# Kernel tuning notes

Measured on AMD Instinct MI355X. Metric: run time of the kernel, lower is better.

## Reference

```python
import jax, jax.numpy as jnp
import numpy as np

N_ITEMS = 30000
N_HOPS = 2
TMP = 0.2
EPS = 1e-12


def _l2norm(x):
    # F.normalize(x, dim=1): x / max(||x||_2, eps)
    n = jnp.sqrt(jnp.sum(x * x, axis=1, keepdims=True))
    return x / jnp.maximum(n, EPS)


def setup_inputs() -> dict:
    key = jax.random.key(0)
    ks = jax.random.split(key, 12)
    n_users, n_entities, n_items, d = 50000, 100000, N_ITEMS, 64
    n_rel, n_fac, n_cls = 16, 4, 8
    n_edges, n_inter = 1000000, 500000
    return {
        'user_emb': jax.random.normal(ks[0], (n_users, d), jnp.float32),
        'entity_emb': jax.random.normal(ks[1], (n_entities, d), jnp.float32),
        'cls_emb': jax.random.normal(ks[2], (n_cls, d), jnp.float32),
        'latent_emb': jax.random.normal(ks[3], (n_fac, d), jnp.float32),
        'relation_emb': jax.random.normal(ks[4], (n_rel, d), jnp.float32),
        'disen_weight_att': jax.random.normal(ks[5], (n_fac, n_rel), jnp.float32),
        'edge_index': jax.random.randint(ks[6], (2, n_edges), 0, n_entities, jnp.int32),
        'edge_type': jax.random.randint(ks[7], (n_edges,), 0, n_rel, jnp.int32),
        'inter_user': jax.random.randint(ks[8], (n_inter,), 0, n_users, jnp.int32),
        'inter_item': jax.random.randint(ks[9], (n_inter,), 0, n_items, jnp.int32),
        'inter_val': jax.random.uniform(ks[10], (n_inter,), jnp.float32),
        'inter_cls': jax.random.randint(ks[11], (n_inter,), 0, n_cls, jnp.int32),
    }


def _cls_aggregate(entity_emb, user_emb, cls_emb, latent_emb, relation_emb,
                   disen_weight_att, edge_index, edge_type,
                   inter_user, inter_item, inter_val, inter_cls,
                   n_users, n_cls):
    n_entities = entity_emb.shape[0]
    item_emb = entity_emb[:N_ITEMS]
    # --- KG aggregate: scatter_mean over head of entity_emb[tail]*rel[edge_type]
    head, tail = edge_index[0], edge_index[1]
    msg = entity_emb[tail] * relation_emb[edge_type]            # [E, d]
    ent_sum = jax.ops.segment_sum(msg, head, num_segments=n_entities)
    cnt = jax.ops.segment_sum(jnp.ones_like(head, jnp.float32), head,
                              num_segments=n_entities)
    entity_agg = ent_sum / jnp.maximum(cnt, 1.0)[:, None]
    # --- user aggregate: sparse interact_mat @ item_emb
    u_msg = inter_val[:, None] * item_emb[inter_item]           # [I, d]
    user_agg = jax.ops.segment_sum(u_msg, inter_user, num_segments=n_users)
    # --- intent attention
    user_disen_att = jax.nn.softmax(user_emb @ latent_emb.T, axis=1)  # [U, F]
    disen_weight = jax.nn.softmax(disen_weight_att, axis=-1) @ relation_emb  # [F, d]
    user_agg = user_disen_att @ disen_weight + user_agg
    # --- class attention: inter_cls_mat[c] @ item_emb for each class
    user_cls_att = jax.nn.softmax(user_emb @ cls_emb.T, axis=1)  # [U, C]
    seg = inter_cls * n_users + inter_user
    user_cls = jax.ops.segment_sum(u_msg, seg, num_segments=n_cls * n_users)
    user_cls = user_cls.reshape(n_cls, n_users, -1)              # [C, U, d]
    user_agg = jnp.einsum('cud,uc->ud', user_cls, user_cls_att) + user_agg
    return entity_agg, user_agg


def _mutual_information(t, temperature):
    nt = _l2norm(t)
    scores = jnp.exp(nt @ nt.T / temperature)
    return -jnp.sum(jnp.log(jnp.diag(scores) / jnp.sum(scores, axis=1)))


def reference(user_emb, entity_emb, cls_emb, latent_emb, relation_emb,
              disen_weight_att, edge_index, edge_type, inter_user,
              inter_item, inter_val, inter_cls):
    n_users = user_emb.shape[0]
    n_cls = cls_emb.shape[0]
    entity_res, user_res = entity_emb, user_emb
    e, u = entity_emb, user_emb
    for _ in range(N_HOPS):
        e, u = _cls_aggregate(e, u, cls_emb, latent_emb, relation_emb,
                              disen_weight_att, edge_index, edge_type,
                              inter_user, inter_item, inter_val, inter_cls,
                              n_users, n_cls)
        e = _l2norm(e)
        u = _l2norm(u)
        entity_res = entity_res + e
        user_res = user_res + u
    cor_loss = _mutual_information(disen_weight_att, TMP)
    return entity_res, user_res, cor_loss
```

## Files before the change

kernel.cpp:

```cpp
#include <hip/hip_runtime.h>
#include <math.h>

typedef unsigned int uint;

constexpr int N_USERS  = 50000;
constexpr int N_ENT    = 100000;
constexpr int D        = 64;
constexpr int N_FAC    = 4;
constexpr int N_CLS    = 8;
constexpr int N_REL    = 16;
constexpr int N_EDGES  = 1000000;
constexpr int N_INTER  = 500000;

constexpr int BSH      = 7;
constexpr int SPB      = 1 << BSH;
constexpr int NBKT_E   = (N_ENT   + SPB - 1) / SPB;
constexpr int NBKT_U   = (N_USERS + SPB - 1) / SPB;
constexpr int CHUNK    = 4096;
constexpr int NB_E     = (N_EDGES + CHUNK - 1) / CHUNK;
constexpr int NB_U     = (N_INTER + CHUNK - 1) / CHUNK;
constexpr int EBUF_CAP = 3072;

constexpr int E_ROWS   = N_ENT + 1;

typedef _Float16 h2_t __attribute__((ext_vector_type(2)));
union U32H2 { uint u; h2_t h; };

__device__ inline float h_lo(uint v) { U32H2 x; x.u = v; return (float)x.h.x; }
__device__ inline float h_hi(uint v) { U32H2 x; x.u = v; return (float)x.h.y; }
__device__ inline uint packh(float a, float b) {
    auto r = __builtin_amdgcn_cvt_pkrtz(a, b);
    union { decltype(r) h; uint u; } x;
    x.h = r;
    return x.u;
}

__device__ inline int wscan64_incl(int x, int lane) {
#pragma unroll
    for (int off = 1; off < 64; off <<= 1) {
        int v = __shfl_up(x, off, 64);
        if (lane >= off) x += v;
    }
    return x;
}

__device__ inline int block_scan_incl(int x, int* wsum) {
    int lane = threadIdx.x & 63, wv = threadIdx.x >> 6;
#pragma unroll
    for (int off = 1; off < 64; off <<= 1) {
        int v = __shfl_up(x, off, 64);
        if (lane >= off) x += v;
    }
    if (lane == 63) wsum[wv] = x;
    __syncthreads();
    if (wv == 0 && lane < 16) {
        int s = wsum[lane];
#pragma unroll
        for (int off = 1; off < 16; off <<= 1) {
            int v = __shfl_up(s, off, 64);
            if (lane >= off) s += v;
        }
        wsum[lane] = s;
    }
    __syncthreads();
    if (wv > 0) x += wsum[wv - 1];
    return x;
}

__global__ void k_convert(const float2* __restrict__ in, uint* __restrict__ out,
                          int n_src, int n_out) {
    for (int i = blockIdx.x * blockDim.x + threadIdx.x; i < n_out;
         i += gridDim.x * blockDim.x) {
        if (i < n_src) {
            float2 v = in[i];
            out[i] = packh(v.x, v.y);
        } else {
            out[i] = 0u;
        }
    }
}

__global__ void k_sort(const int* __restrict__ headE, const int* __restrict__ tailE,
                       const int* __restrict__ etype,
                       const int* __restrict__ iu, const int* __restrict__ ii,
                       const int* __restrict__ icls, const float* __restrict__ ival,
                       uint2* __restrict__ stagE, int* __restrict__ GE, int* __restrict__ RE,
                       uint2* __restrict__ stagU, int* __restrict__ GU, int* __restrict__ RU) {
    __shared__ int hist[NBKT_E];
    __shared__ int soff[NBKT_E + 1];
    __shared__ int cursor[NBKT_E];
    __shared__ int wsum[16];
    __shared__ uint2 sorted[CHUNK];
    int bid = blockIdx.x;
    bool isE = bid < NB_E;
    int blk  = isE ? bid : bid - NB_E;
    int n    = isE ? N_EDGES : N_INTER;
    int nbkt = isE ? NBKT_E : NBKT_U;
    int base = blk * CHUNK;
    int end  = min(base + CHUNK, n);
    int cblk = end - base;

    for (int b = threadIdx.x; b < nbkt; b += 256) hist[b] = 0;
    __syncthreads();

    uint2 ent[16]; int ebk[16];
#pragma unroll
    for (int j = 0; j < 16; ++j) {
        int i = base + threadIdx.x + j * 256;
        ebk[j] = -1;
        if (i < end) {
            uint x, y; int b;
            if (isE) {
                int h = headE[i];
                x = (uint)h; y = (uint)((tailE[i] << 4) | etype[i]); b = h >> BSH;
            } else {
                int u = iu[i];
                x = (uint)((u << 15) | ii[i]);
                y = (__float_as_uint(ival[i]) & ~7u) | (uint)icls[i];
                b = u >> BSH;
            }
            ent[j] = make_uint2(x, y); ebk[j] = b;
            atomicAdd(&hist[b], 1);
        }
    }
    __syncthreads();

    int b0 = threadIdx.x * 4;
    int lsum[4]; int mysum = 0;
#pragma unroll
    for (int j = 0; j < 4; ++j) {
        int b = b0 + j;
        int v = (b < nbkt) ? hist[b] : 0;
        lsum[j] = mysum; mysum += v;
    }
    int excl = block_scan_incl(mysum, wsum) - mysum;
#pragma unroll
    for (int j = 0; j < 4; ++j) {
        int b = b0 + j;
        if (b < nbkt) soff[b] = excl + lsum[j];
    }
    if (threadIdx.x == 0) soff[nbkt] = cblk;
    __syncthreads();
    for (int b = threadIdx.x; b < nbkt; b += 256) cursor[b] = soff[b];
    __syncthreads();

#pragma unroll
    for (int j = 0; j < 16; ++j) {
        if (ebk[j] >= 0) {
            int p = atomicAdd(&cursor[ebk[j]], 1);
            sorted[p] = ent[j];
        }
    }
    __syncthreads();

    uint2* stag = isE ? stagE : stagU;
    int* G = isE ? GE : GU;
    int* R = isE ? RE : RU;
    for (int i = threadIdx.x; i < cblk; i += 256) stag[blk * CHUNK + i] = sorted[i];
    for (int b = threadIdx.x; b < nbkt; b += 256) G[blk * nbkt + b] = hist[b];
    for (int b = threadIdx.x; b <= nbkt; b += 256) R[blk * (nbkt + 1) + b] = soff[b];
}

__global__ void k_bscanA(int* __restrict__ GE, int* __restrict__ totE,
                         int* __restrict__ GU, int* __restrict__ totU) {
    int bid = blockIdx.x;
    bool isE = bid < NBKT_E;
    int bkt  = isE ? bid : bid - NBKT_E;
    int NB   = isE ? NB_E : NB_U;
    int nbkt = isE ? NBKT_E : NBKT_U;
    int* G   = isE ? GE : GU;
    int* tot = isE ? totE : totU;
    int l = threadIdx.x;
    int carry = 0;
    for (int base = 0; base < NB; base += 64) {
        int x = (base + l < NB) ? G[(base + l) * nbkt + bkt] : 0;
        int incl = wscan64_incl(x, l);
        if (base + l < NB) G[(base + l) * nbkt + bkt] = carry + incl - x;
        carry += __shfl(incl, 63, 64);
    }
    if (l == 0) tot[bkt] = carry;
}

__device__ inline void scan_tot(const int* __restrict__ tot, int* __restrict__ base,
                                int nbkt, int l, int* __restrict__ off_last, int nseg) {
    int carry = 0;
    for (int b = 0; b < nbkt; b += 64) {
        int x = (b + l < nbkt) ? tot[b + l] : 0;
        int incl = wscan64_incl(x, l);
        if (b + l < nbkt) base[b + l] = carry + incl - x;
        carry += __shfl(incl, 63, 64);
    }
    if (l == 0) {
        base[nbkt] = carry;
        off_last[nseg] = carry;
        off_last[nseg + 1] = carry;
    }
}

__global__ void k_bscanB(const int* __restrict__ totE, int* __restrict__ baseE,
                         const int* __restrict__ totU, int* __restrict__ baseU,
                         int* __restrict__ eoff, int* __restrict__ uoff) {
    int t = threadIdx.x;
    if (t < 64) scan_tot(totE, baseE, NBKT_E, t, eoff, N_ENT);
    else        scan_tot(totU, baseU, NBKT_U, t - 64, uoff, N_USERS);
}

__global__ void k_final(const uint2* __restrict__ stagE, const int* __restrict__ GE,
                        const int* __restrict__ RE, const int* __restrict__ baseE,
                        const uint2* __restrict__ stagU, const int* __restrict__ GU,
                        const int* __restrict__ RU, const int* __restrict__ baseU,
                        int* __restrict__ eoff, int* __restrict__ uoff,
                        int* __restrict__ epay, int2* __restrict__ ipv) {
    __shared__ uint2 ebuf[EBUF_CAP];
    __shared__ int cnt[SPB], soff[SPB], cur[SPB];
    int bid = blockIdx.x;
    bool isE = bid < NBKT_E;
    int bkt = bid < NBKT_E ? bid : bid - NBKT_E;
    const uint2* stag = isE ? stagE : stagU;
    const int* G  = isE ? GE : GU;
    const int* R  = isE ? RE : RU;
    const int* bb = isE ? baseE : baseU;
    int* off      = isE ? eoff : uoff;
    int NB   = isE ? NB_E : NB_U;
    int nbkt = isE ? NBKT_E : NBKT_U;
    int nseg = isE ? N_ENT : N_USERS;
    int r0 = bb[bkt], r1 = bb[bkt + 1];
    int bsz = r1 - r0;
    int t = threadIdx.x;
    if (t < SPB) cnt[t] = 0;
    for (int blk = t; blk < NB; blk += 256) {
        int rs  = R[blk * (nbkt + 1) + bkt];
        int re  = R[blk * (nbkt + 1) + bkt + 1];
        int dst = G[blk * nbkt + bkt];
        for (int j = rs; j < re; ++j) {
            int d = dst + (j - rs);
            if (d < EBUF_CAP) ebuf[d] = stag[blk * CHUNK + j];
        }
    }
    __syncthreads();
    for (int i = t; i < bsz; i += 256) {
        uint2 e = ebuf[i];
        int s = (int)(isE ? e.x : (e.x >> 15)) & (SPB - 1);
        atomicAdd(&cnt[s], 1);
    }
    __syncthreads();
    if (t < 64) {
        int a0 = cnt[2 * t], a1 = cnt[2 * t + 1];
        int incl = wscan64_incl(a0 + a1, t);
        int excl = incl - (a0 + a1);
        soff[2 * t] = excl;
        soff[2 * t + 1] = excl + a0;
    }
    __syncthreads();
    if (t < SPB) {
        cur[t] = soff[t];
        int seg = bkt * SPB + t;
        if (seg < nseg) off[seg] = r0 + soff[t];
    }
    __syncthreads();
    for (int i = t; i < bsz; i += 256) {
        uint2 e = ebuf[i];
        int s = (int)(isE ? e.x : (e.x >> 15)) & (SPB - 1);
        int pos = r0 + atomicAdd(&cur[s], 1);
        if (isE) {
            epay[pos] = (int)e.y;
        } else {
            int item = (int)(e.x & 0x7FFF), cls = (int)(e.y & 7u);
            ipv[pos] = make_int2((item << 3) | cls, (int)(e.y & ~7u));
        }
    }
}

__global__ void k_dw_loss(const float* __restrict__ datt,
                          const float* __restrict__ rel,
                          float* __restrict__ dw,
                          float* __restrict__ loss_out,
                          uint4* __restrict__ relh4) {
    __shared__ float p[N_FAC][N_REL];
    __shared__ float nrm[N_FAC];
    __shared__ float sc[N_FAC][N_FAC];
    int t = threadIdx.x;
    for (int s = t; s < N_REL * 8; s += 64) {
        int r = s >> 3, kk = s & 7;
        const float* rp = rel + r * 64 + kk * 8;
        relh4[s] = make_uint4(packh(rp[0], rp[1]), packh(rp[2], rp[3]),
                              packh(rp[4], rp[5]), packh(rp[6], rp[7]));
    }
    if (t < N_FAC) {
        float m = -1e30f;
        for (int r = 0; r < N_REL; ++r) m = fmaxf(m, datt[t * N_REL + r]);
        float tmp[N_REL]; float s = 0.f;
        for (int r = 0; r < N_REL; ++r) { tmp[r] = expf(datt[t * N_REL + r] - m); s += tmp[r]; }
        for (int r = 0; r < N_REL; ++r) p[t][r] = tmp[r] / s;
        float ss = 0.f;
        for (int r = 0; r < N_REL; ++r) { float v = datt[t * N_REL + r]; ss += v * v; }
        nrm[t] = fmaxf(sqrtf(ss), 1e-12f);
    }
    __syncthreads();
    if (t < D) {
        for (int f = 0; f < N_FAC; ++f) {
            float acc = 0.f;
            for (int r = 0; r < N_REL; ++r) acc += p[f][r] * rel[r * D + t];
            dw[f * D + t] = acc;
        }
    }
    if (t < N_FAC * N_FAC) {
        int i = t >> 2, j = t & 3;
        float s = 0.f;
        for (int r = 0; r < N_REL; ++r) s += datt[i * N_REL + r] * datt[j * N_REL + r];
        s /= nrm[i] * nrm[j];
        sc[i][j] = expf(s * 5.0f);
    }
    __syncthreads();
    if (t == 0) {
        float loss = 0.f;
        for (int i = 0; i < N_FAC; ++i) {
            float rowsum = 0.f;
            for (int j = 0; j < N_FAC; ++j) rowsum += sc[i][j];
            loss += logf(sc[i][i] / rowsum);
        }
        *loss_out = -loss;
    }
}

template<bool F16>
__global__ void k_user_att(const void* __restrict__ uin,
                           const float* __restrict__ latent,
                           const float* __restrict__ cls,
                           float* __restrict__ att4,
                           float* __restrict__ att8) {
    int gid = blockIdx.x * blockDim.x + threadIdx.x;
    int row = gid >> 4;
    int lane = gid & 15;
    if (row >= N_USERS) return;
    float4 uv;
    if (F16) {
        uint2 q = ((const uint2*)uin)[row * 16 + lane];
        uv.x = h_lo(q.x); uv.y = h_hi(q.x); uv.z = h_lo(q.y); uv.w = h_hi(q.y);
    } else {
        uv = ((const float4*)uin)[row * 16 + lane];
    }
    float dots[12];
#pragma unroll
    for (int f = 0; f < 4; ++f) {
        float4 lv = ((const float4*)latent)[f * 16 + lane];
        dots[f] = uv.x*lv.x + uv.y*lv.y + uv.z*lv.z + uv.w*lv.w;
    }
#pragma unroll
    for (int c = 0; c < 8; ++c) {
        float4 cv = ((const float4*)cls)[c * 16 + lane];
        dots[4+c] = uv.x*cv.x + uv.y*cv.y + uv.z*cv.z + uv.w*cv.w;
    }
#pragma unroll
    for (int j = 0; j < 12; ++j) {
        float v = dots[j];
        for (int m = 1; m < 16; m <<= 1) v += __shfl_xor(v, m, 16);
        dots[j] = v;
    }
    float m4 = fmaxf(fmaxf(dots[0], dots[1]), fmaxf(dots[2], dots[3]));
    float e4v[4]; float s4 = 0.f;
#pragma unroll
    for (int f = 0; f < 4; ++f) { e4v[f] = expf(dots[f] - m4); s4 += e4v[f]; }
    float m8 = dots[4];
#pragma unroll
    for (int c = 1; c < 8; ++c) m8 = fmaxf(m8, dots[4+c]);
    float e8v[8]; float s8 = 0.f;
#pragma unroll
    for (int c = 0; c < 8; ++c) { e8v[c] = expf(dots[4+c] - m8); s8 += e8v[c]; }
    if (lane < 4) {
        float v = e4v[0];
#pragma unroll
        for (int f = 1; f < 4; ++f) if (lane == f) v = e4v[f];
        att4[row * 4 + lane] = v / s4;
    }
    if (lane < 8) {
        float v = e8v[0];
#pragma unroll
        for (int c = 1; c < 8; ++c) if (lane == c) v = e8v[c];
        att8[row * 8 + lane] = v / s8;
    }
}

__global__ __launch_bounds__(256)
void k_hop(const uint4* __restrict__ etab,
           const float4* __restrict__ entbase,
           const float4* __restrict__ usrbase,
           const uint4* __restrict__ relh4,
           const int* __restrict__ eoff,
           const int* __restrict__ epay,
           const int* __restrict__ uoff,
           const int2* __restrict__ ipv,
           const float* __restrict__ att4,
           const float* __restrict__ att8,
           const float4* __restrict__ dw4,
           uint4* __restrict__ stateE,
           uint4* __restrict__ stateU,
           float4* __restrict__ outE,
           float4* __restrict__ outU,
           int mode) {
    int gid = blockIdx.x * 256 + threadIdx.x;
    int gw = gid >> 3;
    int k = threadIdx.x & 7;
    if (gw >= E_ROWS + N_USERS) return;
    bool isEnt = gw < E_ROWS;
    float a0 = 0.f, a1 = 0.f, a2 = 0.f, a3 = 0.f;
    float a4 = 0.f, a5 = 0.f, a6 = 0.f, a7 = 0.f;

    if (isEnt) {
        int w = gw;
        int beg = eoff[w], end = eoff[w + 1];
        int nE = end - beg;
        const int* pp = epay + beg;
        int pc[8];
#pragma unroll
        for (int q = 0; q < 8; ++q) pc[q] = pp[q];
        for (int bse = 0; bse < nE; bse += 8) {
            int c = nE - bse;
            int pn[8];
#pragma unroll
            for (int q = 0; q < 8; ++q) pn[q] = pp[bse + 8 + q];
            uint4 ev[8], rl[8];
#pragma unroll
            for (int q = 0; q < 8; ++q) {
                int p = (q < c) ? pc[q] : (N_ENT << 4);
                ev[q] = etab[(((size_t)(p >> 4)) << 3) + k];
                rl[q] = relh4[((p & 15) << 3) + k];
            }
#pragma unroll
            for (int q = 0; q < 8; ++q) {
                a0 = fmaf(h_lo(ev[q].x), h_lo(rl[q].x), a0);
                a1 = fmaf(h_hi(ev[q].x), h_hi(rl[q].x), a1);
                a2 = fmaf(h_lo(ev[q].y), h_lo(rl[q].y), a2);
                a3 = fmaf(h_hi(ev[q].y), h_hi(rl[q].y), a3);
                a4 = fmaf(h_lo(ev[q].z), h_lo(rl[q].z), a4);
                a5 = fmaf(h_hi(ev[q].z), h_hi(rl[q].z), a5);
                a6 = fmaf(h_lo(ev[q].w), h_lo(rl[q].w), a6);
                a7 = fmaf(h_hi(ev[q].w), h_hi(rl[q].w), a7);
            }
#pragma unroll
            for (int q = 0; q < 8; ++q) pc[q] = pn[q];
        }
        float ss = a0*a0 + a1*a1 + a2*a2 + a3*a3 + a4*a4 + a5*a5 + a6*a6 + a7*a7;
#pragma unroll
        for (int m = 1; m < 8; m <<= 1) ss += __shfl_xor(ss, m, 8);
        float s = 1.0f / fmaxf(sqrtf(ss), 1e-12f);
        float v0 = a0*s, v1 = a1*s, v2 = a2*s, v3 = a3*s;
        float v4 = a4*s, v5 = a5*s, v6 = a6*s, v7 = a7*s;
        if (mode == 0) {
            stateE[((size_t)w << 3) + k] =
                make_uint4(packh(v0, v1), packh(v2, v3), packh(v4, v5), packh(v6, v7));
        } else if (w < N_ENT) {
            size_t b = ((size_t)w << 4) + (k << 1);
            float4 b0 = entbase[b], b1 = entbase[b + 1];
            uint4 own = etab[((size_t)w << 3) + k];
            float4 o0 = make_float4(b0.x + h_lo(own.x) + v0, b0.y + h_hi(own.x) + v1,
                                    b0.z + h_lo(own.y) + v2, b0.w + h_hi(own.y) + v3);
            float4 o1 = make_float4(b1.x + h_lo(own.z) + v4, b1.y + h_hi(own.z) + v5,
                                    b1.z + h_lo(own.w) + v6, b1.w + h_hi(own.w) + v7);
            outE[b] = o0; outE[b + 1] = o1;
        }
    } else {
        int w = gw - E_ROWS;
        int beg = uoff[w], end = uoff[w + 1];
        int nE = end - beg;
        const int2* pv = ipv + beg;
        float a8v = att8[w * 8 + k];
        int2 ec[8];
#pragma unroll
        for (int q = 0; q < 8; ++q) ec[q] = pv[q];
        for (int bse = 0; bse < nE; bse += 8) {
            int c = nE - bse;
            int2 en[8];
#pragma unroll
            for (int q = 0; q < 8; ++q) en[q] = pv[bse + 8 + q];
            uint4 ev[8]; float wg[8];
#pragma unroll
            for (int q = 0; q < 8; ++q) {
                int p = ec[q].x;
                int pe = (q < c) ? p : 0;
                ev[q] = etab[(((size_t)(pe >> 3)) << 3) + k];
                float wgt = __int_as_float(ec[q].y) * (1.0f + __shfl(a8v, p & 7, 8));
                wg[q] = (q < c) ? wgt : 0.0f;
            }
#pragma unroll
            for (int q = 0; q < 8; ++q) {
                a0 = fmaf(h_lo(ev[q].x), wg[q], a0);
                a1 = fmaf(h_hi(ev[q].x), wg[q], a1);
                a2 = fmaf(h_lo(ev[q].y), wg[q], a2);
                a3 = fmaf(h_hi(ev[q].y), wg[q], a3);
                a4 = fmaf(h_lo(ev[q].z), wg[q], a4);
                a5 = fmaf(h_hi(ev[q].z), wg[q], a5);
                a6 = fmaf(h_lo(ev[q].w), wg[q], a6);
                a7 = fmaf(h_hi(ev[q].w), wg[q], a7);
            }
#pragma unroll
            for (int q = 0; q < 8; ++q) ec[q] = en[q];
        }
#pragma unroll
        for (int f = 0; f < 4; ++f) {
            float a = att4[w * 4 + f];
            const float4* dd = dw4 + f * 16 + (k << 1);
            float4 d0 = dd[0], d1 = dd[1];
            a0 = fmaf(a, d0.x, a0); a1 = fmaf(a, d0.y, a1);
            a2 = fmaf(a, d0.z, a2); a3 = fmaf(a, d0.w, a3);
            a4 = fmaf(a, d1.x, a4); a5 = fmaf(a, d1.y, a5);
            a6 = fmaf(a, d1.z, a6); a7 = fmaf(a, d1.w, a7);
        }
        float ss = a0*a0 + a1*a1 + a2*a2 + a3*a3 + a4*a4 + a5*a5 + a6*a6 + a7*a7;
#pragma unroll
        for (int m = 1; m < 8; m <<= 1) ss += __shfl_xor(ss, m, 8);
        float s = 1.0f / fmaxf(sqrtf(ss), 1e-12f);
        float v0 = a0*s, v1 = a1*s, v2 = a2*s, v3 = a3*s;
        float v4 = a4*s, v5 = a5*s, v6 = a6*s, v7 = a7*s;
        if (mode == 0) {
            stateU[((size_t)w << 3) + k] =
                make_uint4(packh(v0, v1), packh(v2, v3), packh(v4, v5), packh(v6, v7));
        } else {
            size_t b = ((size_t)w << 4) + (k << 1);
            float4 b0 = usrbase[b], b1 = usrbase[b + 1];
            uint4 own = stateU[((size_t)w << 3) + k];
            float4 o0 = make_float4(b0.x + h_lo(own.x) + v0, b0.y + h_hi(own.x) + v1,
                                    b0.z + h_lo(own.y) + v2, b0.w + h_hi(own.y) + v3);
            float4 o1 = make_float4(b1.x + h_lo(own.z) + v4, b1.y + h_hi(own.z) + v5,
                                    b1.z + h_lo(own.w) + v6, b1.w + h_hi(own.w) + v7);
            outU[b] = o0; outU[b + 1] = o1;
        }
    }
}

extern "C" void kernel_launch(void* const* d_in, const int* in_sizes, int n_in,
                              void* d_out, int out_size, void* d_ws, size_t ws_size,
                              hipStream_t stream) {
    const float* user_emb   = (const float*)d_in[0];
    const float* entity_emb = (const float*)d_in[1];
    const float* cls_emb    = (const float*)d_in[2];
    const float* latent_emb = (const float*)d_in[3];
    const float* rel_emb    = (const float*)d_in[4];
    const float* disen      = (const float*)d_in[5];
    const int*   edge_index = (const int*)d_in[6];
    const int*   edge_type  = (const int*)d_in[7];
    const int*   inter_user = (const int*)d_in[8];
    const int*   inter_item = (const int*)d_in[9];
    const float* inter_val  = (const float*)d_in[10];
    const int*   inter_cls  = (const int*)d_in[11];

    float* out      = (float*)d_out;
    float* out_ent  = out;
    float* out_user = out + (size_t)N_ENT * D;
    float* out_loss = out + (size_t)N_ENT * D + (size_t)N_USERS * D;

    char* w = (char*)d_ws;
    auto alloc = [&](size_t bytes) -> char* {
        char* p = w;
        w += (bytes + 255) & ~(size_t)255;
        return p;
    };
    uint*  ebuf0 = (uint*)alloc((size_t)E_ROWS * 32 * 4);
    uint*  eA    = (uint*)alloc((size_t)E_ROWS * 32 * 4);
    uint*  uA    = (uint*)alloc((size_t)N_USERS * 32 * 4);
    int*   epay  = (int*)alloc((size_t)(N_EDGES + 32) * 4);
    int2*  ipv   = (int2*)alloc((size_t)(N_INTER + 32) * 8);
    int*   eoff  = (int*)alloc((size_t)(N_ENT + 4) * 4);
    int*   uoff  = (int*)alloc((size_t)(N_USERS + 4) * 4);
    int*   GE    = (int*)alloc((size_t)NB_E * NBKT_E * 4);
    int*   RE    = (int*)alloc((size_t)NB_E * (NBKT_E + 1) * 4);
    int*   GU    = (int*)alloc((size_t)NB_U * NBKT_U * 4);
    int*   RU    = (int*)alloc((size_t)NB_U * (NBKT_U + 1) * 4);
    int*   totE  = (int*)alloc((size_t)NBKT_E * 4);
    int*   totU  = (int*)alloc((size_t)NBKT_U * 4);
    int*   baseE = (int*)alloc((size_t)(NBKT_E + 1) * 4);
    int*   baseU = (int*)alloc((size_t)(NBKT_U + 1) * 4);
    uint4* relh  = (uint4*)alloc((size_t)N_REL * 8 * 16);
    float* att4  = (float*)alloc((size_t)N_USERS * N_FAC * 4);
    float* att8  = (float*)alloc((size_t)N_USERS * N_CLS * 4);
    float* dw    = (float*)alloc((size_t)N_FAC * D * 4);

    uint2* stagE = (uint2*)eA;
    uint2* stagU = (uint2*)uA;

    const int* head = edge_index;
    const int* tail = edge_index + N_EDGES;

    k_convert<<<2048, 256, 0, stream>>>((const float2*)entity_emb, ebuf0,
                                        N_ENT * 32, E_ROWS * 32);
    k_dw_loss<<<1, 64, 0, stream>>>(disen, rel_emb, dw, out_loss, relh);

    k_sort  <<<NB_E + NB_U, 256, 0, stream>>>(head, tail, edge_type,
                                              inter_user, inter_item, inter_cls, inter_val,
                                              stagE, GE, RE, stagU, GU, RU);
    k_bscanA<<<NBKT_E + NBKT_U, 64, 0, stream>>>(GE, totE, GU, totU);
    k_bscanB<<<1, 128, 0, stream>>>(totE, baseE, totU, baseU, eoff, uoff);
    k_final <<<NBKT_E + NBKT_U, 256, 0, stream>>>(stagE, GE, RE, baseE,
                                                  stagU, GU, RU, baseU,
                                                  eoff, uoff, epay, ipv);

    const int att_blocks = (N_USERS * 16 + 255) / 256;
    const int hop_blocks = ((E_ROWS + N_USERS) * 8 + 255) / 256;

    k_user_att<false><<<att_blocks, 256, 0, stream>>>(user_emb, latent_emb, cls_emb, att4, att8);
    k_hop<<<hop_blocks, 256, 0, stream>>>((const uint4*)ebuf0, nullptr, nullptr,
                                          relh, eoff, epay, uoff, ipv,
                                          att4, att8, (const float4*)dw,
                                          (uint4*)eA, (uint4*)uA, nullptr, nullptr, 0);

    k_user_att<true><<<att_blocks, 256, 0, stream>>>(uA, latent_emb, cls_emb, att4, att8);
    k_hop<<<hop_blocks, 256, 0, stream>>>((const uint4*)eA,
                                          (const float4*)entity_emb, (const float4*)user_emb,
                                          relh, eoff, epay, uoff, ipv,
                                          att4, att8, (const float4*)dw,
                                          nullptr, (uint4*)uA,
                                          (float4*)out_ent, (float4*)out_user, 1);
}
```

Before: 149.8 us.

## Fuse user attention into hop kernel and merge small setup kernels

The per-user softmax attention over latent factors and classes is now computed inside the hop kernel from the user's current embedding, so the separate attention kernels and their att4/att8 global buffers go away. The dw and loss computation is folded into the last block of the conversion kernel. The two bucket-scan kernels become one, where the last block to finish, found with an atomic counter and thread fences, does the final scan. The aim is fewer launches and less global traffic, at the cost of extra register pressure in the hop kernel and a last-block synchronisation pattern that depends on the counter being reset every call.

```diff
diff --git a/kernel.cpp b/kernel.cpp
--- a/kernel.cpp
+++ b/kernel.cpp
@@ -67,10 +67,65 @@
     return x;
 }
 
-__global__ void k_convert(const float2* __restrict__ in, uint* __restrict__ out,
-                          int n_src, int n_out) {
-    for (int i = blockIdx.x * blockDim.x + threadIdx.x; i < n_out;
-         i += gridDim.x * blockDim.x) {
+__global__ void k_cvt_dw(const float2* __restrict__ in, uint* __restrict__ out,
+                         int n_src, int n_out,
+                         const float* __restrict__ datt,
+                         const float* __restrict__ rel,
+                         float* __restrict__ dw,
+                         float* __restrict__ loss_out,
+                         uint4* __restrict__ relh4,
+                         int* __restrict__ done_ctr) {
+    __shared__ float p[N_FAC][N_REL];
+    __shared__ float nrm[N_FAC];
+    __shared__ float sc[N_FAC][N_FAC];
+    int t = threadIdx.x;
+    if (blockIdx.x == gridDim.x - 1) {
+        if (t == 0) *done_ctr = 0;
+        for (int s = t; s < N_REL * 8; s += 256) {
+            int r = s >> 3, kk = s & 7;
+            const float* rp = rel + r * 64 + kk * 8;
+            relh4[s] = make_uint4(packh(rp[0], rp[1]), packh(rp[2], rp[3]),
+                                  packh(rp[4], rp[5]), packh(rp[6], rp[7]));
+        }
+        if (t < N_FAC) {
+            float m = -1e30f;
+            for (int r = 0; r < N_REL; ++r) m = fmaxf(m, datt[t * N_REL + r]);
+            float tmp[N_REL]; float s = 0.f;
+            for (int r = 0; r < N_REL; ++r) { tmp[r] = expf(datt[t * N_REL + r] - m); s += tmp[r]; }
+            for (int r = 0; r < N_REL; ++r) p[t][r] = tmp[r] / s;
+            float ss = 0.f;
+            for (int r = 0; r < N_REL; ++r) { float v = datt[t * N_REL + r]; ss += v * v; }
+            nrm[t] = fmaxf(sqrtf(ss), 1e-12f);
+        }
+        __syncthreads();
+        if (t < D) {
+            for (int f = 0; f < N_FAC; ++f) {
+                float acc = 0.f;
+                for (int r = 0; r < N_REL; ++r) acc += p[f][r] * rel[r * D + t];
+                dw[f * D + t] = acc;
+            }
+        }
+        if (t < N_FAC * N_FAC) {
+            int i = t >> 2, j = t & 3;
+            float s = 0.f;
+            for (int r = 0; r < N_REL; ++r) s += datt[i * N_REL + r] * datt[j * N_REL + r];
+            s /= nrm[i] * nrm[j];
+            sc[i][j] = expf(s * 5.0f);
+        }
+        __syncthreads();
+        if (t == 0) {
+            float loss = 0.f;
+            for (int i = 0; i < N_FAC; ++i) {
+                float rowsum = 0.f;
+                for (int j = 0; j < N_FAC; ++j) rowsum += sc[i][j];
+                loss += logf(sc[i][i] / rowsum);
+            }
+            *loss_out = -loss;
+        }
+        return;
+    }
+    int nb = gridDim.x - 1;
+    for (int i = blockIdx.x * 256 + t; i < n_out; i += nb * 256) {
         if (i < n_src) {
             float2 v = in[i];
             out[i] = packh(v.x, v.y);
@@ -161,8 +216,27 @@
     for (int b = threadIdx.x; b <= nbkt; b += 256) R[blk * (nbkt + 1) + b] = soff[b];
 }
 
-__global__ void k_bscanA(int* __restrict__ GE, int* __restrict__ totE,
-                         int* __restrict__ GU, int* __restrict__ totU) {
+__device__ inline void scan_tot(const int* __restrict__ tot, int* __restrict__ base,
+                                int nbkt, int l, int* __restrict__ off_last, int nseg) {
+    int carry = 0;
+    for (int b = 0; b < nbkt; b += 64) {
+        int x = (b + l < nbkt) ? tot[b + l] : 0;
+        int incl = wscan64_incl(x, l);
+        if (b + l < nbkt) base[b + l] = carry + incl - x;
+        carry += __shfl(incl, 63, 64);
+    }
+    if (l == 0) {
+        base[nbkt] = carry;
+        off_last[nseg] = carry;
+        off_last[nseg + 1] = carry;
+    }
+}
+
+__global__ void k_bscan(int* __restrict__ GE, int* __restrict__ totE,
+                        int* __restrict__ GU, int* __restrict__ totU,
+                        int* __restrict__ baseE, int* __restrict__ baseU,
+                        int* __restrict__ eoff, int* __restrict__ uoff,
+                        int* __restrict__ done_ctr) {
     int bid = blockIdx.x;
     bool isE = bid < NBKT_E;
     int bkt  = isE ? bid : bid - NBKT_E;
@@ -179,30 +253,15 @@
         carry += __shfl(incl, 63, 64);
     }
     if (l == 0) tot[bkt] = carry;
-}
-
-__device__ inline void scan_tot(const int* __restrict__ tot, int* __restrict__ base,
-                                int nbkt, int l, int* __restrict__ off_last, int nseg) {
-    int carry = 0;
-    for (int b = 0; b < nbkt; b += 64) {
-        int x = (b + l < nbkt) ? tot[b + l] : 0;
-        int incl = wscan64_incl(x, l);
-        if (b + l < nbkt) base[b + l] = carry + incl - x;
-        carry += __shfl(incl, 63, 64);
-    }
-    if (l == 0) {
-        base[nbkt] = carry;
-        off_last[nseg] = carry;
-        off_last[nseg + 1] = carry;
-    }
-}
-
-__global__ void k_bscanB(const int* __restrict__ totE, int* __restrict__ baseE,
-                         const int* __restrict__ totU, int* __restrict__ baseU,
-                         int* __restrict__ eoff, int* __restrict__ uoff) {
-    int t = threadIdx.x;
-    if (t < 64) scan_tot(totE, baseE, NBKT_E, t, eoff, N_ENT);
-    else        scan_tot(totU, baseU, NBKT_U, t - 64, uoff, N_USERS);
+    __threadfence();
+    __shared__ int amlast;
+    if (l == 0) amlast = (atomicAdd(done_ctr, 1) == NBKT_E + NBKT_U - 1);
+    __syncthreads();
+    if (amlast) {
+        __threadfence();
+        scan_tot(totE, baseE, NBKT_E, l, eoff, N_ENT);
+        scan_tot(totU, baseU, NBKT_U, l, uoff, N_USERS);
+    }
 }
 
 __global__ void k_final(const uint2* __restrict__ stagE, const int* __restrict__ GE,
@@ -271,133 +330,24 @@
     }
 }
 
-__global__ void k_dw_loss(const float* __restrict__ datt,
-                          const float* __restrict__ rel,
-                          float* __restrict__ dw,
-                          float* __restrict__ loss_out,
-                          uint4* __restrict__ relh4) {
-    __shared__ float p[N_FAC][N_REL];
-    __shared__ float nrm[N_FAC];
-    __shared__ float sc[N_FAC][N_FAC];
-    int t = threadIdx.x;
-    for (int s = t; s < N_REL * 8; s += 64) {
-        int r = s >> 3, kk = s & 7;
-        const float* rp = rel + r * 64 + kk * 8;
-        relh4[s] = make_uint4(packh(rp[0], rp[1]), packh(rp[2], rp[3]),
-                              packh(rp[4], rp[5]), packh(rp[6], rp[7]));
-    }
-    if (t < N_FAC) {
-        float m = -1e30f;
-        for (int r = 0; r < N_REL; ++r) m = fmaxf(m, datt[t * N_REL + r]);
-        float tmp[N_REL]; float s = 0.f;
-        for (int r = 0; r < N_REL; ++r) { tmp[r] = expf(datt[t * N_REL + r] - m); s += tmp[r]; }
-        for (int r = 0; r < N_REL; ++r) p[t][r] = tmp[r] / s;
-        float ss = 0.f;
-        for (int r = 0; r < N_REL; ++r) { float v = datt[t * N_REL + r]; ss += v * v; }
-        nrm[t] = fmaxf(sqrtf(ss), 1e-12f);
-    }
-    __syncthreads();
-    if (t < D) {
-        for (int f = 0; f < N_FAC; ++f) {
-            float acc = 0.f;
-            for (int r = 0; r < N_REL; ++r) acc += p[f][r] * rel[r * D + t];
-            dw[f * D + t] = acc;
-        }
-    }
-    if (t < N_FAC * N_FAC) {
-        int i = t >> 2, j = t & 3;
-        float s = 0.f;
-        for (int r = 0; r < N_REL; ++r) s += datt[i * N_REL + r] * datt[j * N_REL + r];
-        s /= nrm[i] * nrm[j];
-        sc[i][j] = expf(s * 5.0f);
-    }
-    __syncthreads();
-    if (t == 0) {
-        float loss = 0.f;
-        for (int i = 0; i < N_FAC; ++i) {
-            float rowsum = 0.f;
-            for (int j = 0; j < N_FAC; ++j) rowsum += sc[i][j];
-            loss += logf(sc[i][i] / rowsum);
-        }
-        *loss_out = -loss;
-    }
-}
-
-template<bool F16>
-__global__ void k_user_att(const void* __restrict__ uin,
-                           const float* __restrict__ latent,
-                           const float* __restrict__ cls,
-                           float* __restrict__ att4,
-                           float* __restrict__ att8) {
-    int gid = blockIdx.x * blockDim.x + threadIdx.x;
-    int row = gid >> 4;
-    int lane = gid & 15;
-    if (row >= N_USERS) return;
-    float4 uv;
-    if (F16) {
-        uint2 q = ((const uint2*)uin)[row * 16 + lane];
-        uv.x = h_lo(q.x); uv.y = h_hi(q.x); uv.z = h_lo(q.y); uv.w = h_hi(q.y);
-    } else {
-        uv = ((const float4*)uin)[row * 16 + lane];
-    }
-    float dots[12];
-#pragma unroll
-    for (int f = 0; f < 4; ++f) {
-        float4 lv = ((const float4*)latent)[f * 16 + lane];
-        dots[f] = uv.x*lv.x + uv.y*lv.y + uv.z*lv.z + uv.w*lv.w;
-    }
-#pragma unroll
-    for (int c = 0; c < 8; ++c) {
-        float4 cv = ((const float4*)cls)[c * 16 + lane];
-        dots[4+c] = uv.x*cv.x + uv.y*cv.y + uv.z*cv.z + uv.w*cv.w;
-    }
-#pragma unroll
-    for (int j = 0; j < 12; ++j) {
-        float v = dots[j];
-        for (int m = 1; m < 16; m <<= 1) v += __shfl_xor(v, m, 16);
-        dots[j] = v;
-    }
-    float m4 = fmaxf(fmaxf(dots[0], dots[1]), fmaxf(dots[2], dots[3]));
-    float e4v[4]; float s4 = 0.f;
-#pragma unroll
-    for (int f = 0; f < 4; ++f) { e4v[f] = expf(dots[f] - m4); s4 += e4v[f]; }
-    float m8 = dots[4];
-#pragma unroll
-    for (int c = 1; c < 8; ++c) m8 = fmaxf(m8, dots[4+c]);
-    float e8v[8]; float s8 = 0.f;
-#pragma unroll
-    for (int c = 0; c < 8; ++c) { e8v[c] = expf(dots[4+c] - m8); s8 += e8v[c]; }
-    if (lane < 4) {
-        float v = e4v[0];
-#pragma unroll
-        for (int f = 1; f < 4; ++f) if (lane == f) v = e4v[f];
-        att4[row * 4 + lane] = v / s4;
-    }
-    if (lane < 8) {
-        float v = e8v[0];
-#pragma unroll
-        for (int c = 1; c < 8; ++c) if (lane == c) v = e8v[c];
-        att8[row * 8 + lane] = v / s8;
-    }
-}
-
+template<int MODE>
 __global__ __launch_bounds__(256)
 void k_hop(const uint4* __restrict__ etab,
            const float4* __restrict__ entbase,
            const float4* __restrict__ usrbase,
+           const uint4* __restrict__ ustate_in,
            const uint4* __restrict__ relh4,
            const int* __restrict__ eoff,
            const int* __restrict__ epay,
            const int* __restrict__ uoff,
            const int2* __restrict__ ipv,
-           const float* __restrict__ att4,
-           const float* __restrict__ att8,
+           const float4* __restrict__ latent4,
+           const float4* __restrict__ cls4,
            const float4* __restrict__ dw4,
-           uint4* __restrict__ stateE,
-           uint4* __restrict__ stateU,
+           uint4* __restrict__ stateE_out,
+           uint4* __restrict__ stateU_out,
            float4* __restrict__ outE,
-           float4* __restrict__ outU,
-           int mode) {
+           float4* __restrict__ outU) {
     int gid = blockIdx.x * 256 + threadIdx.x;
     int gw = gid >> 3;
     int k = threadIdx.x & 7;
@@ -446,8 +396,8 @@
         float s = 1.0f / fmaxf(sqrtf(ss), 1e-12f);
         float v0 = a0*s, v1 = a1*s, v2 = a2*s, v3 = a3*s;
         float v4 = a4*s, v5 = a5*s, v6 = a6*s, v7 = a7*s;
-        if (mode == 0) {
-            stateE[((size_t)w << 3) + k] =
+        if (MODE == 0) {
+            stateE_out[((size_t)w << 3) + k] =
                 make_uint4(packh(v0, v1), packh(v2, v3), packh(v4, v5), packh(v6, v7));
         } else if (w < N_ENT) {
             size_t b = ((size_t)w << 4) + (k << 1);
@@ -464,7 +414,48 @@
         int beg = uoff[w], end = uoff[w + 1];
         int nE = end - beg;
         const int2* pv = ipv + beg;
-        float a8v = att8[w * 8 + k];
+
+        float u0, u1, u2, u3, u4, u5, u6, u7;
+        uint4 own;
+        if (MODE == 0) {
+            size_t bb = ((size_t)w << 4) + (k << 1);
+            float4 x0 = usrbase[bb], x1 = usrbase[bb + 1];
+            u0 = x0.x; u1 = x0.y; u2 = x0.z; u3 = x0.w;
+            u4 = x1.x; u5 = x1.y; u6 = x1.z; u7 = x1.w;
+        } else {
+            own = ustate_in[((size_t)w << 3) + k];
+            u0 = h_lo(own.x); u1 = h_hi(own.x); u2 = h_lo(own.y); u3 = h_hi(own.y);
+            u4 = h_lo(own.z); u5 = h_hi(own.z); u6 = h_lo(own.w); u7 = h_hi(own.w);
+        }
+        float d[12];
+#pragma unroll
+        for (int f = 0; f < 12; ++f) {
+            const float4* lp = (f < 4 ? latent4 + f * 16 : cls4 + (f - 4) * 16) + (k << 1);
+            float4 l0 = lp[0], l1 = lp[1];
+            d[f] = u0*l0.x + u1*l0.y + u2*l0.z + u3*l0.w
+                 + u4*l1.x + u5*l1.y + u6*l1.z + u7*l1.w;
+        }
+#pragma unroll
+        for (int j = 0; j < 12; ++j) {
+#pragma unroll
+            for (int off = 1; off < 8; off <<= 1) d[j] += __shfl_xor(d[j], off, 8);
+        }
+        float m4 = fmaxf(fmaxf(d[0], d[1]), fmaxf(d[2], d[3]));
+        float e40 = expf(d[0] - m4), e41 = expf(d[1] - m4);
+        float e42 = expf(d[2] - m4), e43 = expf(d[3] - m4);
+        float r4 = 1.0f / (e40 + e41 + e42 + e43);
+        float af0 = e40 * r4, af1 = e41 * r4, af2 = e42 * r4, af3 = e43 * r4;
+        float m8 = d[4];
+#pragma unroll
+        for (int c = 1; c < 8; ++c) m8 = fmaxf(m8, d[4 + c]);
+        float e8[8]; float s8 = 0.f;
+#pragma unroll
+        for (int c = 0; c < 8; ++c) { e8[c] = expf(d[4 + c] - m8); s8 += e8[c]; }
+        float a8e = e8[0];
+#pragma unroll
+        for (int c = 1; c < 8; ++c) if (k == c) a8e = e8[c];
+        float a8v = a8e / s8;
+
         int2 ec[8];
 #pragma unroll
         for (int q = 0; q < 8; ++q) ec[q] = pv[q];
@@ -498,7 +489,7 @@
         }
 #pragma unroll
         for (int f = 0; f < 4; ++f) {
-            float a = att4[w * 4 + f];
+            float a = (f == 0) ? af0 : (f == 1) ? af1 : (f == 2) ? af2 : af3;
             const float4* dd = dw4 + f * 16 + (k << 1);
             float4 d0 = dd[0], d1 = dd[1];
             a0 = fmaf(a, d0.x, a0); a1 = fmaf(a, d0.y, a1);
@@ -512,13 +503,12 @@
         float s = 1.0f / fmaxf(sqrtf(ss), 1e-12f);
         float v0 = a0*s, v1 = a1*s, v2 = a2*s, v3 = a3*s;
         float v4 = a4*s, v5 = a5*s, v6 = a6*s, v7 = a7*s;
-        if (mode == 0) {
-            stateU[((size_t)w << 3) + k] =
+        if (MODE == 0) {
+            stateU_out[((size_t)w << 3) + k] =
                 make_uint4(packh(v0, v1), packh(v2, v3), packh(v4, v5), packh(v6, v7));
         } else {
             size_t b = ((size_t)w << 4) + (k << 1);
             float4 b0 = usrbase[b], b1 = usrbase[b + 1];
-            uint4 own = stateU[((size_t)w << 3) + k];
             float4 o0 = make_float4(b0.x + h_lo(own.x) + v0, b0.y + h_hi(own.x) + v1,
                                     b0.z + h_lo(own.y) + v2, b0.w + h_hi(own.y) + v3);
             float4 o1 = make_float4(b1.x + h_lo(own.z) + v4, b1.y + h_hi(own.z) + v5,
@@ -571,9 +561,8 @@
     int*   baseE = (int*)alloc((size_t)(NBKT_E + 1) * 4);
     int*   baseU = (int*)alloc((size_t)(NBKT_U + 1) * 4);
     uint4* relh  = (uint4*)alloc((size_t)N_REL * 8 * 16);
-    float* att4  = (float*)alloc((size_t)N_USERS * N_FAC * 4);
-    float* att8  = (float*)alloc((size_t)N_USERS * N_CLS * 4);
     float* dw    = (float*)alloc((size_t)N_FAC * D * 4);
+    int*   dctr  = (int*)alloc(256);
 
     uint2* stagE = (uint2*)eA;
     uint2* stagU = (uint2*)uA;
@@ -581,33 +570,37 @@
     const int* head = edge_index;
     const int* tail = edge_index + N_EDGES;
 
-    k_convert<<<2048, 256, 0, stream>>>((const float2*)entity_emb, ebuf0,
-                                        N_ENT * 32, E_ROWS * 32);
-    k_dw_loss<<<1, 64, 0, stream>>>(disen, rel_emb, dw, out_loss, relh);
-
-    k_sort  <<<NB_E + NB_U, 256, 0, stream>>>(head, tail, edge_type,
-                                              inter_user, inter_item, inter_cls, inter_val,
-                                              stagE, GE, RE, stagU, GU, RU);
-    k_bscanA<<<NBKT_E + NBKT_U, 64, 0, stream>>>(GE, totE, GU, totU);
-    k_bscanB<<<1, 128, 0, stream>>>(totE, baseE, totU, baseU, eoff, uoff);
-    k_final <<<NBKT_E + NBKT_U, 256, 0, stream>>>(stagE, GE, RE, baseE,
-                                                  stagU, GU, RU, baseU,
-                                                  eoff, uoff, epay, ipv);
-
-    const int att_blocks = (N_USERS * 16 + 255) / 256;
+    k_cvt_dw<<<2048, 256, 0, stream>>>((const float2*)entity_emb, ebuf0,
+                                       N_ENT * 32, E_ROWS * 32,
+                                       disen, rel_emb, dw, out_loss, relh, dctr);
+    k_sort <<<NB_E + NB_U, 256, 0, stream>>>(head, tail, edge_type,
+                                             inter_user, inter_item, inter_cls, inter_val,
+                                             stagE, GE, RE, stagU, GU, RU);
+    k_bscan<<<NBKT_E + NBKT_U, 64, 0, stream>>>(GE, totE, GU, totU,
+                                                baseE, baseU, eoff, uoff, dctr);
+    k_final<<<NBKT_E + NBKT_U, 256, 0, stream>>>(stagE, GE, RE, baseE,
+                                                 stagU, GU, RU, baseU,
+                                                 eoff, uoff, epay, ipv);
+
     const int hop_blocks = ((E_ROWS + N_USERS) * 8 + 255) / 256;
 
-    k_user_att<false><<<att_blocks, 256, 0, stream>>>(user_emb, latent_emb, cls_emb, att4, att8);
-    k_hop<<<hop_blocks, 256, 0, stream>>>((const uint4*)ebuf0, nullptr, nullptr,
-                                          relh, eoff, epay, uoff, ipv,
-                                          att4, att8, (const float4*)dw,
-                                          (uint4*)eA, (uint4*)uA, nullptr, nullptr, 0);
-
-    k_user_att<true><<<att_blocks, 256, 0, stream>>>(uA, latent_emb, cls_emb, att4, att8);
-    k_hop<<<hop_blocks, 256, 0, stream>>>((const uint4*)eA,
-                                          (const float4*)entity_emb, (const float4*)user_emb,
-                                          relh, eoff, epay, uoff, ipv,
-                                          att4, att8, (const float4*)dw,
-                                          nullptr, (uint4*)uA,
-                                          (float4*)out_ent, (float4*)out_user, 1);
-}
+    k_hop<0><<<hop_blocks, 256, 0, stream>>>((const uint4*)ebuf0, nullptr,
+                                             (const float4*)user_emb, nullptr,
+                                             relh, eoff, epay, uoff, ipv,
+                                             (const float4*)latent_emb,
+                                             (const float4*)cls_emb,
+                                             (const float4*)dw,
+                                             (uint4*)eA, (uint4*)uA,
+                                             nullptr, nullptr);
+
+    k_hop<1><<<hop_blocks, 256, 0, stream>>>((const uint4*)eA,
+                                             (const float4*)entity_emb,
+                                             (const float4*)user_emb,
+                                             (const uint4*)uA,
+                                             relh, eoff, epay, uoff, ipv,
+                                             (const float4*)latent_emb,
+                                             (const float4*)cls_emb,
+                                             (const float4*)dw,
+                                             nullptr, nullptr,
+                                             (float4*)out_ent, (float4*)out_user);
+}
```

After: 209.3 us. 1.4x slower.
